# Performance work log

Hardware: AMD Instinct MI355X
Metric: run time of the kernel (lower is better)

Reference implementation:

```python
import jax, jax.numpy as jnp
import numpy as np

NH = 4          # num_heads
EPS = 1e-6
GATE_CAP = 15.0
LOGIT_CAP = 30.0


def soft_cap(x, cap):
    return cap * jnp.tanh(x / cap)


def rms_norm(x, w, eps=EPS):
    xf = x.astype(jnp.float32)
    scale = jax.lax.rsqrt(jnp.mean(xf * xf, axis=-1, keepdims=True) + eps)
    return (xf * scale).astype(x.dtype) * w


def multihead_layernorm(h, w, eps=EPS):
    # h: [B, NH, S, DH]; LayerNorm over DH per head, weight over NH*DH
    hf = h.astype(jnp.float32)
    mu = jnp.mean(hf, axis=-1, keepdims=True)
    var = jnp.mean((hf - mu) ** 2, axis=-1, keepdims=True)
    hn = ((hf - mu) * jax.lax.rsqrt(var + eps)).astype(h.dtype)
    B, nh, S, DH = h.shape
    hn = hn.transpose(0, 2, 1, 3).reshape(B, S, nh * DH)  # [B,S,v_dim]
    return hn * w


def mlstm_parallel(q, k, v, i_pre, f_pre, eps=EPS):
    # q,k: [B,NH,S,Dqk]; v: [B,NH,S,Dv]; i_pre,f_pre: [B,NH,S]
    S = q.shape[2]
    dqk = q.shape[-1]
    logf = jax.nn.log_sigmoid(f_pre.astype(jnp.float32))      # [B,NH,S]
    F = jnp.cumsum(logf, axis=-1)
    # logD[t,s] = F[t] - F[s] + i[s]  for s <= t
    logD = F[..., :, None] - F[..., None, :] + i_pre.astype(jnp.float32)[..., None, :]
    mask = jnp.tril(jnp.ones((S, S), dtype=bool))
    logD = jnp.where(mask, logD, -jnp.inf)
    m = jnp.max(logD, axis=-1, keepdims=True)                  # [B,NH,S,1]
    Dmat = jnp.exp(logD - m)
    scores = jnp.einsum('bhsd,bhtd->bhst', q, k) / jnp.sqrt(float(dqk))
    C = scores * Dmat                                          # [B,NH,S,S]
    n = jnp.maximum(jnp.abs(C.sum(-1)), jnp.exp(-m[..., 0]))   # [B,NH,S]
    h = jnp.einsum('bhst,bhtd->bhsd', C, v) / (n[..., None] + eps)
    return h


def block(x, p):
    (n1, wq, wk, wv, wog, wi, bi, wf, bf, mhw, wout, n2, wg, wu, wd) = p
    B, S, D = x.shape
    xm = rms_norm(x, n1)
    q = xm @ wq.T
    k = xm @ wk.T
    v = xm @ wv.T
    o_pre = xm @ wog.T
    i_pre = soft_cap(xm @ wi.T + bi, GATE_CAP)   # [B,S,NH]
    f_pre = soft_cap(xm @ wf.T + bf, GATE_CAP)
    q = q.reshape(B, S, NH, -1).transpose(0, 2, 1, 3)
    k = k.reshape(B, S, NH, -1).transpose(0, 2, 1, 3)
    v = v.reshape(B, S, NH, -1).transpose(0, 2, 1, 3)
    h = mlstm_parallel(q, k, v, i_pre.transpose(0, 2, 1), f_pre.transpose(0, 2, 1))
    hn = multihead_layernorm(h, mhw)             # [B,S,v_dim]
    y = (hn * jax.nn.sigmoid(o_pre)) @ wout.T
    x = x + y
    xf = rms_norm(x, n2)
    ff = (jax.nn.silu(xf @ wg.T) * (xf @ wu.T)) @ wd.T
    return x + ff


def setup_inputs() -> dict:
    key = jax.random.key(0)
    ks = jax.random.split(key, 16)
    L, D, V, UP, QK = 2, 1024, 32000, 2752, 512
    s = 0.02
    return {
        'tokens': jax.random.randint(ks[0], (1, 2048), 0, V),
        'emb': jax.random.normal(ks[1], (V, D)) * s,
        'norm1_w': jnp.ones((L, D)),
        'Wq': jax.random.normal(ks[2], (L, QK, D)) * s,
        'Wk': jax.random.normal(ks[3], (L, QK, D)) * s,
        'Wv': jax.random.normal(ks[4], (L, D, D)) * s,
        'Wog': jax.random.normal(ks[5], (L, D, D)) * s,
        'Wi': jax.random.normal(ks[6], (L, NH, D)) * s,
        'bi': jax.random.normal(ks[7], (L, NH)) * s,
        'Wf': jax.random.normal(ks[8], (L, NH, D)) * s,
        'bf': jnp.ones((L, NH)) * 3.0,
        'mh_w': jnp.ones((L, D)),
        'Wout': jax.random.normal(ks[9], (L, D, D)) * s,
        'norm2_w': jnp.ones((L, D)),
        'Wg': jax.random.normal(ks[10], (L, UP, D)) * s,
        'Wu': jax.random.normal(ks[11], (L, UP, D)) * s,
        'Wd': jax.random.normal(ks[12], (L, D, UP)) * s,
        'out_norm_w': jnp.ones((D,)),
        'Wlm': jax.random.normal(ks[13], (V, D)) * s,
    }


def reference(tokens, emb, norm1_w, Wq, Wk, Wv, Wog, Wi, bi, Wf, bf, mh_w,
              Wout, norm2_w, Wg, Wu, Wd, out_norm_w, Wlm):
    x = emb[tokens]                    # [B,S,D]
    L = Wq.shape[0]
    for l in range(L):
        p = (norm1_w[l], Wq[l], Wk[l], Wv[l], Wog[l], Wi[l], bi[l], Wf[l],
             bf[l], mh_w[l], Wout[l], norm2_w[l], Wg[l], Wu[l], Wd[l])
        x = block(x, p)
    x = rms_norm(x, out_norm_w)
    logits = x @ Wlm.T
    return soft_cap(logits, LOGIT_CAP)
```

## Files before the change

kernel.cpp:

```cpp
#include <hip/hip_runtime.h>
#include <hip/hip_bf16.h>
#include <math.h>


#define S_LEN 2048
#define DMODEL 1024
#define WLAYER 12845056

typedef __attribute__((ext_vector_type(8))) __bf16 bf16x8;
typedef __attribute__((ext_vector_type(8))) unsigned short u16x8;
typedef __attribute__((ext_vector_type(4))) unsigned short u16x4;
typedef __attribute__((ext_vector_type(4))) float f32x4v;

union cvu { u16x8 u; bf16x8 b; };

__device__ __forceinline__ unsigned short bf_us(float f) {
  union { __bf16 b; unsigned short u; } c;
  c.b = (__bf16)f;
  return c.u;
}
__device__ __forceinline__ float us_f(unsigned short u) {
  union { __bf16 b; unsigned short u; } c;
  c.u = u;
  return (float)c.b;
}
__device__ __forceinline__ bf16x8 ld_bf8(const unsigned short* p, int byte_off) {
  cvu c;
  c.u = *(const u16x8*)((const char*)p + byte_off);
  return c.b;
}
__device__ __forceinline__ float fast_sigmoid(float v) {
  return 1.0f / (1.0f + __expf(-v));
}
__device__ __forceinline__ float fast_softcap30(float v) {
  float e = __expf(-fabsf(v) * (1.0f / 15.0f));
  float t = (1.0f - e) / (1.0f + e);
  return copysignf(30.0f * t, v);
}

#define AS_G __attribute__((address_space(1)))
#define AS_L __attribute__((address_space(3)))

__device__ __forceinline__ void stage64(const unsigned short* gbase, int K,
                                        unsigned short* lds, int wave, int lane, int k0) {
#pragma unroll
  for (int j = 0; j < 4; ++j) {
    const int rbase = (j * 4 + wave) * 8;
    const int r = rbase + (lane >> 3);
    const int cg = (lane & 7) ^ (r & 7);
    const unsigned short* src = gbase + (size_t)r * K + k0 + cg * 8;
    __builtin_amdgcn_global_load_lds((const AS_G void*)src,
                                     (AS_L void*)(lds + rbase * 64), 16, 0, 0);
  }
}

__device__ __forceinline__ void stage32(const unsigned short* gbase, int K,
                                        unsigned short* lds, int wave, int lane, int k0) {
#pragma unroll
  for (int j = 0; j < 2; ++j) {
    const int r = j * 64 + wave * 16 + (lane >> 2);
    const int cg = (lane & 3) ^ ((r >> 1) & 3);
    const unsigned short* src = gbase + (size_t)r * K + k0 + cg * 8;
    __builtin_amdgcn_global_load_lds((const AS_G void*)src,
                                     (AS_L void*)(lds + (j * 64 + wave * 16) * 32), 16, 0, 0);
  }
}

__global__ __launch_bounds__(256) void embed_kernel(
    const int* __restrict__ tok, const float* __restrict__ emb, float* __restrict__ x) {
  int s = blockIdx.x;
  int t = tok[s];
  const float4 v = *(const float4*)(emb + (size_t)t * DMODEL + threadIdx.x * 4);
  *(float4*)(x + (size_t)s * DMODEL + threadIdx.x * 4) = v;
}

__global__ __launch_bounds__(256) void rmsnorm_kernel(
    const float* __restrict__ x, const float* __restrict__ w,
    unsigned short* __restrict__ outb) {
  int s = blockIdx.x, tid = threadIdx.x;
  const float* xr = x + (size_t)s * DMODEL;
  float4 v = *(const float4*)(xr + tid * 4);
  float ss = v.x * v.x + v.y * v.y + v.z * v.z + v.w * v.w;
#pragma unroll
  for (int off = 32; off > 0; off >>= 1) ss += __shfl_down(ss, off);
  __shared__ float red[4];
  if ((tid & 63) == 0) red[tid >> 6] = ss;
  __syncthreads();
  float tot = red[0] + red[1] + red[2] + red[3];
  float scale = rsqrtf(tot * (1.0f / DMODEL) + 1e-6f);
  float4 wv = *(const float4*)(w + tid * 4);
  u16x4 ub;
  ub[0] = bf_us(v.x * scale * wv.x);
  ub[1] = bf_us(v.y * scale * wv.y);
  ub[2] = bf_us(v.z * scale * wv.z);
  ub[3] = bf_us(v.w * scale * wv.w);
  *(u16x4*)(outb + (size_t)s * DMODEL + tid * 4) = ub;
}

__global__ __launch_bounds__(256) void wcvt8_kernel(
    const float* __restrict__ Wq, const float* __restrict__ Wk,
    const float* __restrict__ Wv, const float* __restrict__ Wog,
    const float* __restrict__ Wout, const float* __restrict__ Wg,
    const float* __restrict__ Wu, const float* __restrict__ Wd,
    const float* __restrict__ Wlm,
    unsigned short* __restrict__ W, unsigned short* __restrict__ Wlm16) {
  const size_t de = ((size_t)blockIdx.x * 256 + threadIdx.x) * 8;
  if (de >= 2ull * WLAYER) {
    size_t i = de - 2ull * WLAYER;
    float4 a0 = *(const float4*)(Wlm + i);
    float4 a1 = *(const float4*)(Wlm + i + 4);
    u16x8 o;
    o[0] = bf_us(a0.x); o[1] = bf_us(a0.y); o[2] = bf_us(a0.z); o[3] = bf_us(a0.w);
    o[4] = bf_us(a1.x); o[5] = bf_us(a1.y); o[6] = bf_us(a1.z); o[7] = bf_us(a1.w);
    *(u16x8*)(Wlm16 + i) = o;
    return;
  }
  int e = (int)de, l = 0;
  if (e >= WLAYER) { l = 1; e -= WLAYER; }
  const float* src = nullptr;
  size_t idx = 0;
  if (e < 524288)       { src = Wq  + (size_t)l * 524288;  idx = e; }
  else if (e < 1048576) { src = Wk  + (size_t)l * 524288;  idx = e - 524288; }
  else if (e < 2097152) { src = Wv  + (size_t)l * 1048576; idx = e - 1048576; }
  else if (e < 3145728) { src = Wog + (size_t)l * 1048576; idx = e - 2097152; }
  else if (e < 4194304) { src = Wout + (size_t)l * 1048576; idx = e - 3145728; }
  else if (e < 7077888) {
    int t = e - 4194304, row = t >> 10;
    if (row < 2752) { src = Wg + (size_t)l * 2818048; idx = t; }
  } else if (e < 9961472) {
    int t = e - 7077888, row = t >> 10;
    if (row < 2752) { src = Wu + (size_t)l * 2818048; idx = t; }
  } else {
    int t = e - 9961472, row = t / 2816, col = t - row * 2816;
    if (col < 2752) { src = Wd + (size_t)l * 2818048; idx = row * 2752 + col; }
  }
  u16x8 o;
  if (src) {
    float4 a0 = *(const float4*)(src + idx);
    float4 a1 = *(const float4*)(src + idx + 4);
    o[0] = bf_us(a0.x); o[1] = bf_us(a0.y); o[2] = bf_us(a0.z); o[3] = bf_us(a0.w);
    o[4] = bf_us(a1.x); o[5] = bf_us(a1.y); o[6] = bf_us(a1.z); o[7] = bf_us(a1.w);
  } else {
#pragma unroll
    for (int k = 0; k < 8; ++k) o[k] = 0;
  }
  *(u16x8*)(W + de) = o;
}

template <int EPI>
__global__ __launch_bounds__(256) void gemm_bb_kernel(
    const unsigned short* __restrict__ A, const unsigned short* __restrict__ B,
    const void* Xv, void* Cv, int K, int ldc) {
  __shared__ __align__(16) unsigned short SH[3 * 8192];
  const int tid = threadIdx.x;
  const int wave = tid >> 6, lane = tid & 63;
  const int gx = gridDim.x;
  const int nwg = gx * gridDim.y;
  const int d = blockIdx.y * gx + blockIdx.x;
  const int q = nwg >> 3;
  const int lgc = (d & 7) * q + (d >> 3);
  const int bm = (lgc % gx) * 128, bn = (lgc / gx) * 128;
  const int wr = (wave >> 1) * 64, wc = (wave & 1) * 64;
  const int lr = lane & 15, lhi = lane >> 4;
  const unsigned short* Ab = A + (size_t)bm * K;
  const unsigned short* Bb = B + (size_t)bn * K;
  f32x4v acc[4][4] = {};

  auto stageT = [&](int tau) {
    unsigned short* base = SH + (tau % 3) * 8192;
    stage32(Ab, K, base, wave, lane, tau * 32);
    stage32(Bb, K, base + 4096, wave, lane, tau * 32);
  };

  const int NT = K >> 5;
  stageT(0);
  stageT(1);
  for (int t = 0; t < NT; ++t) {
    if (t < NT - 1) asm volatile("s_waitcnt vmcnt(4)" ::: "memory");
    else            asm volatile("s_waitcnt vmcnt(0)" ::: "memory");
    asm volatile("s_barrier" ::: "memory");
    if (t + 2 < NT) stageT(t + 2);
    const unsigned short* Al = SH + (t % 3) * 8192;
    const unsigned short* Bl = Al + 4096;
    bf16x8 af[4], bfr[4];
#pragma unroll
    for (int mi = 0; mi < 4; ++mi) {
      int row = wr + mi * 16 + lr;
      af[mi] = *(const bf16x8*)&Al[row * 32 + ((lhi ^ ((row >> 1) & 3)) << 3)];
    }
#pragma unroll
    for (int ni = 0; ni < 4; ++ni) {
      int row = wc + ni * 16 + lr;
      bfr[ni] = *(const bf16x8*)&Bl[row * 32 + ((lhi ^ ((row >> 1) & 3)) << 3)];
    }
    __builtin_amdgcn_s_setprio(1);
#pragma unroll
    for (int mi = 0; mi < 4; ++mi)
#pragma unroll
      for (int ni = 0; ni < 4; ++ni)
        acc[mi][ni] = __builtin_amdgcn_mfma_f32_16x16x32_bf16(af[mi], bfr[ni], acc[mi][ni], 0, 0, 0);
    __builtin_amdgcn_s_setprio(0);
  }
#pragma unroll
  for (int mi = 0; mi < 4; ++mi) {
#pragma unroll
    for (int ni = 0; ni < 4; ++ni) {
#pragma unroll
      for (int j = 0; j < 4; ++j) {
        int row = bm + wr + mi * 16 + lhi * 4 + j;
        int col = bn + wc + ni * 16 + lr;
        float v = acc[mi][ni][j];
        if (EPI == 0)
          ((float*)Cv)[(size_t)row * ldc + col] = v;
        if (EPI == 1)
          ((float*)Cv)[(size_t)row * ldc + col] = v + ((const float*)Xv)[(size_t)row * ldc + col];
      }
    }
  }
}

__global__ __launch_bounds__(512, 2) void lm256_kernel(
    const unsigned short* __restrict__ A, const unsigned short* __restrict__ B,
    float* __restrict__ C) {
  __shared__ __align__(16) unsigned short SH[3 * 16384];
  const int K = 1024, N = 32000, NT = 32;
  const int tid = threadIdx.x;
  const int wave = tid >> 6, lane = tid & 63;
  const int lr = lane & 15, lg = lane >> 4;
  const int wm = wave >> 2, wn = wave & 3;
  const int d = blockIdx.y * 8 + blockIdx.x;
  const int lgc = (d & 7) * 125 + (d >> 3);
  const int bm = (lgc & 7) * 256;
  const int bn = (lgc >> 3) * 256;
  const unsigned short* Ab = A + (size_t)bm * K;
  const unsigned short* Bb = B + (size_t)bn * K;

  auto stageM = [&](const unsigned short* gbase, unsigned short* lds, int k0) {
#pragma unroll
    for (int j = 0; j < 2; ++j) {
      const int r = j * 128 + wave * 16 + (lane >> 2);
      const int cg = (lane & 3) ^ ((r >> 1) & 3);
      const unsigned short* src = gbase + (size_t)r * K + k0 + cg * 8;
      __builtin_amdgcn_global_load_lds((const AS_G void*)src,
                                       (AS_L void*)(lds + (j * 128 + wave * 16) * 32), 16, 0, 0);
    }
  };
  auto stageT = [&](int tau) {
    unsigned short* base = SH + (tau % 3) * 16384;
    stageM(Ab, base, tau * 32);
    stageM(Bb, base + 8192, tau * 32);
  };

  f32x4v acc[8][4] = {};
  stageT(0);
  stageT(1);
  for (int t = 0; t < NT; ++t) {
    if (t < NT - 1) asm volatile("s_waitcnt vmcnt(4)" ::: "memory");
    else            asm volatile("s_waitcnt vmcnt(0)" ::: "memory");
    asm volatile("s_barrier" ::: "memory");
    if (t + 2 < NT) stageT(t + 2);
    const unsigned short* Al = SH + (t % 3) * 16384;
    const unsigned short* Bl = Al + 8192;
    bf16x8 bfr[4];
#pragma unroll
    for (int ni = 0; ni < 4; ++ni) {
      int row = wn * 64 + ni * 16 + lr;
      bfr[ni] = *(const bf16x8*)&Bl[row * 32 + ((lg ^ ((row >> 1) & 3)) << 3)];
    }
#pragma unroll
    for (int mi = 0; mi < 8; ++mi) {
      int row = wm * 128 + mi * 16 + lr;
      bf16x8 af = *(const bf16x8*)&Al[row * 32 + ((lg ^ ((row >> 1) & 3)) << 3)];
      __builtin_amdgcn_s_setprio(1);
#pragma unroll
      for (int ni = 0; ni < 4; ++ni)
        acc[mi][ni] = __builtin_amdgcn_mfma_f32_16x16x32_bf16(af, bfr[ni], acc[mi][ni], 0, 0, 0);
      __builtin_amdgcn_s_setprio(0);
    }
  }
#pragma unroll
  for (int mi = 0; mi < 8; ++mi)
#pragma unroll
    for (int ni = 0; ni < 4; ++ni)
#pragma unroll
      for (int jj = 0; jj < 4; ++jj) {
        int row = bm + wm * 128 + mi * 16 + lg * 4 + jj;
        int col = bn + wn * 64 + ni * 16 + lr;
        C[(size_t)row * N + col] = fast_softcap30(acc[mi][ni][jj]);
      }
}

__global__ __launch_bounds__(256) void qkvo_kernel(
    const unsigned short* __restrict__ A, const unsigned short* __restrict__ Wq16,
    const unsigned short* __restrict__ Wk16, const unsigned short* __restrict__ Wv16,
    const unsigned short* __restrict__ Wog16,
    unsigned short* __restrict__ qb, unsigned short* __restrict__ kb,
    unsigned short* __restrict__ vTb, float* __restrict__ og) {
  __shared__ __align__(16) unsigned short SH[3 * 8192];
  const int tid = threadIdx.x;
  const int wave = tid >> 6, lane = tid & 63;
  const int gx = gridDim.x;
  const int nwg = gx * gridDim.y;
  const int dd = blockIdx.y * gx + blockIdx.x;
  const int qq = nwg >> 3;
  const int lgc = (dd & 7) * qq + (dd >> 3);
  const int bm = (lgc % gx) * 128;
  const int by = lgc / gx;
  const unsigned short* B;
  int bnl, mode;
  if (by < 4)       { B = Wq16;  bnl = by * 128;        mode = 0; }
  else if (by < 8)  { B = Wk16;  bnl = (by - 4) * 128;  mode = 1; }
  else if (by < 16) { B = Wv16;  bnl = (by - 8) * 128;  mode = 2; }
  else              { B = Wog16; bnl = (by - 16) * 128; mode = 3; }
  const int K = 1024;
  const int wr = (wave >> 1) * 64, wc = (wave & 1) * 64;
  const int lr = lane & 15, lhi = lane >> 4;
  const unsigned short* Ab = A + (size_t)bm * K;
  const unsigned short* Bb = B + (size_t)bnl * K;
  f32x4v acc[4][4] = {};

  auto stageT = [&](int tau) {
    unsigned short* base = SH + (tau % 3) * 8192;
    stage32(Ab, K, base, wave, lane, tau * 32);
    stage32(Bb, K, base + 4096, wave, lane, tau * 32);
  };

  const int NT = 32;
  stageT(0);
  stageT(1);
  for (int t = 0; t < NT; ++t) {
    if (t < NT - 1) asm volatile("s_waitcnt vmcnt(4)" ::: "memory");
    else            asm volatile("s_waitcnt vmcnt(0)" ::: "memory");
    asm volatile("s_barrier" ::: "memory");
    if (t + 2 < NT) stageT(t + 2);
    const unsigned short* Al = SH + (t % 3) * 8192;
    const unsigned short* Bl = Al + 4096;
    bf16x8 af[4], bfr[4];
#pragma unroll
    for (int mi = 0; mi < 4; ++mi) {
      int row = wr + mi * 16 + lr;
      af[mi] = *(const bf16x8*)&Al[row * 32 + ((lhi ^ ((row >> 1) & 3)) << 3)];
    }
#pragma unroll
    for (int ni = 0; ni < 4; ++ni) {
      int row = wc + ni * 16 + lr;
      bfr[ni] = *(const bf16x8*)&Bl[row * 32 + ((lhi ^ ((row >> 1) & 3)) << 3)];
    }
    __builtin_amdgcn_s_setprio(1);
#pragma unroll
    for (int mi = 0; mi < 4; ++mi)
#pragma unroll
      for (int ni = 0; ni < 4; ++ni)
        acc[mi][ni] = __builtin_amdgcn_mfma_f32_16x16x32_bf16(af[mi], bfr[ni], acc[mi][ni], 0, 0, 0);
    __builtin_amdgcn_s_setprio(0);
  }
  if (mode == 2) {
    __syncthreads();
#pragma unroll
    for (int mi = 0; mi < 4; ++mi)
#pragma unroll
      for (int ni = 0; ni < 4; ++ni)
#pragma unroll
        for (int j = 0; j < 4; ++j) {
          int row = wr + mi * 16 + lhi * 4 + j;
          int col = wc + ni * 16 + lr;
          int byte = col * 256 + ((((row >> 3) ^ (col & 7)) << 4)) + (row & 7) * 2;
          *(unsigned short*)((char*)SH + byte) = bf_us(acc[mi][ni][j]);
        }
    __syncthreads();
#pragma unroll
    for (int i = 0; i < 8; ++i) {
      int c = i * 16 + (tid >> 4);
      int rg = tid & 15;
      u16x8 u = *(const u16x8*)((const char*)SH + c * 256 + ((rg ^ (c & 7)) << 4));
      *(u16x8*)(vTb + (size_t)(bnl + c) * S_LEN + bm + rg * 8) = u;
    }
  } else {
#pragma unroll
    for (int mi = 0; mi < 4; ++mi)
#pragma unroll
      for (int ni = 0; ni < 4; ++ni)
#pragma unroll
        for (int j = 0; j < 4; ++j) {
          int row = bm + wr + mi * 16 + lhi * 4 + j;
          int col = bnl + wc + ni * 16 + lr;
          if (mode == 0)      qb[(size_t)row * 512 + col] = bf_us(acc[mi][ni][j]);
          else if (mode == 1) kb[(size_t)row * 512 + col] = bf_us(acc[mi][ni][j]);
          else                og[(size_t)row * 1024 + col] = acc[mi][ni][j];
        }
  }
}

__global__ __launch_bounds__(256) void ffn_kernel(
    const unsigned short* __restrict__ A, const unsigned short* __restrict__ Bg,
    const unsigned short* __restrict__ Bu, unsigned short* __restrict__ Gb) {
  __shared__ __align__(16) unsigned short As[128 * 64];
  __shared__ __align__(16) unsigned short Bgs[128 * 64];
  __shared__ __align__(16) unsigned short Bus[128 * 64];
  const int K = 1024;
  const int tid = threadIdx.x;
  const int wave = tid >> 6, lane = tid & 63;
  const int gx = gridDim.x;
  const int nwg = gx * gridDim.y;
  const int dd = blockIdx.y * gx + blockIdx.x;
  const int qq = nwg >> 3;
  const int lgc = (dd & 7) * qq + (dd >> 3);
  const int bm = (lgc % gx) * 128;
  const int bn = (lgc / gx) * 128;
  const int wr = (wave >> 1) * 64, wc = (wave & 1) * 64;
  const int lr = lane & 15, lhi = lane >> 4;
  const unsigned short* Ab = A + (size_t)bm * K;
  const unsigned short* Bgb = Bg + (size_t)bn * K;
  const unsigned short* Bub = Bu + (size_t)bn * K;
  f32x4v accg[4][4] = {};
  f32x4v accu[4][4] = {};
  for (int it = 0; it < 16; ++it) {
    stage64(Ab, K, As, wave, lane, it << 6);
    stage64(Bgb, K, Bgs, wave, lane, it << 6);
    stage64(Bub, K, Bus, wave, lane, it << 6);
    __syncthreads();
#pragma unroll
    for (int kk = 0; kk < 2; ++kk) {
      const int sw = (((kk * 4 + lhi) ^ (lr & 7)) << 3);
      bf16x8 af[4], bg[4], bu[4];
#pragma unroll
      for (int mi = 0; mi < 4; ++mi) af[mi] = *(const bf16x8*)&As[(wr + mi * 16 + lr) * 64 + sw];
#pragma unroll
      for (int ni = 0; ni < 4; ++ni) bg[ni] = *(const bf16x8*)&Bgs[(wc + ni * 16 + lr) * 64 + sw];
#pragma unroll
      for (int ni = 0; ni < 4; ++ni) bu[ni] = *(const bf16x8*)&Bus[(wc + ni * 16 + lr) * 64 + sw];
#pragma unroll
      for (int mi = 0; mi < 4; ++mi)
#pragma unroll
        for (int ni = 0; ni < 4; ++ni) {
          accg[mi][ni] = __builtin_amdgcn_mfma_f32_16x16x32_bf16(af[mi], bg[ni], accg[mi][ni], 0, 0, 0);
          accu[mi][ni] = __builtin_amdgcn_mfma_f32_16x16x32_bf16(af[mi], bu[ni], accu[mi][ni], 0, 0, 0);
        }
    }
    __syncthreads();
  }
#pragma unroll
  for (int mi = 0; mi < 4; ++mi) {
#pragma unroll
    for (int ni = 0; ni < 4; ++ni) {
#pragma unroll
      for (int j = 0; j < 4; ++j) {
        int row = bm + wr + mi * 16 + lhi * 4 + j;
        int col = bn + wc + ni * 16 + lr;
        float g = accg[mi][ni][j];
        float sv = g * fast_sigmoid(g) * accu[mi][ni][j];
        Gb[(size_t)row * 2816 + col] = bf_us(sv);
      }
    }
  }
}

__global__ __launch_bounds__(256) void gates_kernel(
    const float* __restrict__ x, const float* __restrict__ n1,
    const float* __restrict__ Wi, const float* __restrict__ bi,
    const float* __restrict__ Wf, const float* __restrict__ bfv,
    float* __restrict__ ipre, float* __restrict__ fpre) {
  int s = blockIdx.x;
  int head = threadIdx.x >> 6, lane = threadIdx.x & 63;
  const float* xr = x + (size_t)s * DMODEL;
  float xv[16];
  float ss = 0.f;
#pragma unroll
  for (int j = 0; j < 16; ++j) { xv[j] = xr[lane + j * 64]; ss += xv[j] * xv[j]; }
#pragma unroll
  for (int off = 32; off > 0; off >>= 1) ss += __shfl_xor(ss, off);
  float scale = rsqrtf(ss * (1.0f / DMODEL) + 1e-6f);
  const float* wi = Wi + head * DMODEL;
  const float* wf = Wf + head * DMODEL;
  float si = 0.f, sf = 0.f;
#pragma unroll
  for (int j = 0; j < 16; ++j) {
    int c = lane + j * 64;
    float xm = xv[j] * scale * n1[c];
    si += xm * wi[c];
    sf += xm * wf[c];
  }
#pragma unroll
  for (int off = 32; off > 0; off >>= 1) {
    si += __shfl_down(si, off);
    sf += __shfl_down(sf, off);
  }
  if (lane == 0) {
    ipre[head * S_LEN + s] = 15.0f * tanhf((si + bi[head]) * (1.0f / 15.0f));
    fpre[head * S_LEN + s] = 15.0f * tanhf((sf + bfv[head]) * (1.0f / 15.0f));
  }
}

__global__ __launch_bounds__(256) void scan_kernel(
    const float* __restrict__ ipre, const float* __restrict__ fpre,
    float* __restrict__ garr, float* __restrict__ Marr, float* __restrict__ earr) {
  const int h = threadIdx.x >> 6;
  const int lane = threadIdx.x & 63;
  const int base = h * S_LEN + lane * 32;
  float lf[32];
  float lsum = 0.f;
#pragma unroll
  for (int e = 0; e < 32; ++e) {
    float f = fpre[base + e];
    float v = fminf(f, 0.f) - log1pf(expf(-fabsf(f)));
    lf[e] = v;
    lsum += v;
  }
  float scan = lsum;
#pragma unroll
  for (int off = 1; off < 64; off <<= 1) {
    float t = __shfl_up(scan, off);
    if (lane >= off) scan += t;
  }
  float F0 = scan - lsum;
  float gv[32];
  float F = F0, lmax = -1e30f;
#pragma unroll
  for (int e = 0; e < 32; ++e) {
    F += lf[e];
    float g = ipre[base + e] - F;
    gv[e] = g;
    lmax = fmaxf(lmax, g);
    garr[base + e] = g;
  }
  float ms = lmax;
#pragma unroll
  for (int off = 1; off < 64; off <<= 1) {
    float t = __shfl_up(ms, off);
    if (lane >= off) ms = fmaxf(ms, t);
  }
  float em = __shfl_up(ms, 1);
  if (lane == 0) em = -1e30f;
  float run = em;
  F = F0;
#pragma unroll
  for (int e = 0; e < 32; ++e) {
    F += lf[e];
    run = fmaxf(run, gv[e]);
    Marr[base + e] = run;
    earr[base + e] = expf(-(F + run));
  }
}

__global__ __launch_bounds__(256) void mlstm_mfma_kernel(
    const unsigned short* __restrict__ Q, const unsigned short* __restrict__ Kb,
    const unsigned short* __restrict__ vT, const float* __restrict__ garr,
    const float* __restrict__ Marr,
    float* __restrict__ hp, float* __restrict__ npart) {
  const int h = blockIdx.y;
  const int T = blockIdx.x;
  const int sp = blockIdx.z;
  float* hpart = hp + (size_t)sp * 2097152;
  const int tid = threadIdx.x;
  const int w = tid >> 6, l = tid & 63;
  const int lr = l & 15, lg = l >> 4;
  const int hbase = h * S_LEN;
  const int sr = tid >> 4;
  const int sc = tid & 15;

  __shared__ __align__(16) unsigned short Ks[64 * 128];
  __shared__ __align__(16) unsigned short Vs[256 * 64];
  __shared__ __align__(16) unsigned short Ps[64 * 64];

  bf16x8 qf[4];
  {
    const unsigned short* qrow = Q + (size_t)(T * 64 + w * 16 + lr) * 512 + h * 128 + lg * 8;
#pragma unroll
    for (int kt = 0; kt < 4; ++kt) {
      cvu c;
      c.u = *(const u16x8*)(qrow + kt * 32);
      qf[kt] = c.b;
    }
  }
  float Mt[4];
#pragma unroll
  for (int j = 0; j < 4; ++j) Mt[j] = Marr[hbase + T * 64 + w * 16 + lg * 4 + j];

  f32x4v pv[16] = {};
  float nacc[4] = {0.f, 0.f, 0.f, 0.f};
  const float rs = 0.08838834764831845f;

  for (int ch = sp; ch <= T; ch += 4) {
    const int s0 = ch * 64;
    __syncthreads();
#pragma unroll
    for (int i = 0; i < 4; ++i) {
      int r = i * 16 + sr;
      u16x8 u = *(const u16x8*)(Kb + (size_t)(s0 + r) * 512 + h * 128 + sc * 8);
      int byte = r * 256 + ((sc * 16) ^ ((r & 7) << 4));
      *(u16x8*)((char*)Ks + byte) = u;
    }
#pragma unroll
    for (int i = 0; i < 16; ++i) {
      int r = i * 16 + sr;
      u16x4 u = *(const u16x4*)(vT + (size_t)(h * 256 + r) * S_LEN + s0 + sc * 4);
      int byte = r * 128 + ((sc * 8) ^ ((r & 7) << 4));
      *(u16x4*)((char*)Vs + byte) = u;
    }
    __syncthreads();
    f32x4v sa[4] = {};
#pragma unroll
    for (int ni = 0; ni < 4; ++ni) {
#pragma unroll
      for (int kt = 0; kt < 4; ++kt) {
        int row = ni * 16 + lr;
        int byte = row * 256 + (((kt * 32 + lg * 8) * 2) ^ ((row & 7) << 4));
        bf16x8 kf = ld_bf8(Ks, byte);
        sa[ni] = __builtin_amdgcn_mfma_f32_16x16x32_bf16(qf[kt], kf, sa[ni], 0, 0, 0);
      }
    }
#pragma unroll
    for (int ni = 0; ni < 4; ++ni) {
      int sl = ni * 16 + lr;
      int sg = s0 + sl;
      float gv = garr[hbase + sg];
#pragma unroll
      for (int j = 0; j < 4; ++j) {
        int tloc = w * 16 + lg * 4 + j;
        int tg = T * 64 + tloc;
        float wgt = (sg <= tg) ? __expf(gv - Mt[j]) : 0.f;
        float val = sa[ni][j] * rs * wgt;
        nacc[j] += val;
        int byte = tloc * 128 + ((sl * 2) ^ ((tloc & 7) << 4));
        *(unsigned short*)((char*)Ps + byte) = bf_us(val);
      }
    }
#pragma unroll
    for (int kt2 = 0; kt2 < 2; ++kt2) {
      int tloc = w * 16 + lr;
      int sb = (kt2 * 32 + lg * 8) * 2;
      bf16x8 pa = ld_bf8(Ps, tloc * 128 + (sb ^ ((tloc & 7) << 4)));
#pragma unroll
      for (int nv = 0; nv < 16; ++nv) {
        int dv = nv * 16 + lr;
        bf16x8 vb = ld_bf8(Vs, dv * 128 + (sb ^ ((dv & 7) << 4)));
        pv[nv] = __builtin_amdgcn_mfma_f32_16x16x32_bf16(pa, vb, pv[nv], 0, 0, 0);
      }
    }
  }
#pragma unroll
  for (int j = 0; j < 4; ++j) {
#pragma unroll
    for (int off = 1; off < 16; off <<= 1) nacc[j] += __shfl_xor(nacc[j], off);
  }
#pragma unroll
  for (int j = 0; j < 4; ++j) {
    int tg = T * 64 + w * 16 + lg * 4 + j;
    if (lr == 0) npart[sp * 8192 + hbase + tg] = nacc[j];
    float* orow = hpart + (size_t)tg * DMODEL + h * 256;
#pragma unroll
    for (int nvt = 0; nvt < 16; ++nvt) orow[nvt * 16 + lr] = pv[nvt][j];
  }
}

__global__ __launch_bounds__(256) void mhln_gate_kernel(
    const float* __restrict__ hp, const float* __restrict__ npart,
    const float* __restrict__ earr, const float* __restrict__ mhw,
    const float* __restrict__ og, unsigned short* __restrict__ gact) {
  int s = blockIdx.x;
  int head = threadIdx.x >> 6, lane = threadIdx.x & 63;
  float n = (npart[head * S_LEN + s] + npart[8192 + head * S_LEN + s]) +
            (npart[16384 + head * S_LEN + s] + npart[24576 + head * S_LEN + s]);
  float nvv = fmaxf(fabsf(n), earr[head * S_LEN + s]);
  float inv = 1.0f / (nvv + 1e-6f);
  const size_t base = (size_t)s * DMODEL + head * 256;
  float vq[4];
#pragma unroll
  for (int qy = 0; qy < 4; ++qy) {
    size_t o = base + qy * 64 + lane;
    vq[qy] = ((hp[o] + hp[o + 2097152]) + (hp[o + 4194304] + hp[o + 6291456])) * inv;
  }
  float sum = vq[0] + vq[1] + vq[2] + vq[3];
#pragma unroll
  for (int off = 32; off > 0; off >>= 1) sum += __shfl_xor(sum, off);
  float mu = sum * (1.0f / 256.0f);
  float d0 = vq[0] - mu, d1 = vq[1] - mu, d2 = vq[2] - mu, d3 = vq[3] - mu;
  float vs = d0 * d0 + d1 * d1 + d2 * d2 + d3 * d3;
#pragma unroll
  for (int off = 32; off > 0; off >>= 1) vs += __shfl_xor(vs, off);
  float rstd = rsqrtf(vs * (1.0f / 256.0f) + 1e-6f);
  float dn[4] = {d0, d1, d2, d3};
#pragma unroll
  for (int qy = 0; qy < 4; ++qy) {
    int c = head * 256 + qy * 64 + lane;
    float ov = og[(size_t)s * DMODEL + c];
    gact[(size_t)s * DMODEL + c] = bf_us(dn[qy] * rstd * mhw[c] * fast_sigmoid(ov));
  }
}

extern "C" void kernel_launch(void* const* d_in, const int* in_sizes, int n_in,
                              void* d_out, int out_size, void* d_ws, size_t ws_size,
                              hipStream_t stream) {
  (void)in_sizes; (void)n_in; (void)out_size; (void)ws_size;
  const int*   tok   = (const int*)d_in[0];
  const float* emb   = (const float*)d_in[1];
  const float* norm1 = (const float*)d_in[2];
  const float* Wq    = (const float*)d_in[3];
  const float* Wk    = (const float*)d_in[4];
  const float* Wv    = (const float*)d_in[5];
  const float* Wog   = (const float*)d_in[6];
  const float* Wi    = (const float*)d_in[7];
  const float* bi    = (const float*)d_in[8];
  const float* Wf    = (const float*)d_in[9];
  const float* bfp   = (const float*)d_in[10];
  const float* mhw   = (const float*)d_in[11];
  const float* Wout  = (const float*)d_in[12];
  const float* norm2 = (const float*)d_in[13];
  const float* Wg    = (const float*)d_in[14];
  const float* Wu    = (const float*)d_in[15];
  const float* Wd    = (const float*)d_in[16];
  const float* onw   = (const float*)d_in[17];
  const float* Wlm   = (const float*)d_in[18];

  char* wsb = (char*)d_ws;
  const size_t MB = 1ull << 20;
  float*          x    = (float*)wsb;
  unsigned short* xmb  = (unsigned short*)(wsb + 8 * MB);
  float*          ipre = (float*)(wsb + 12 * MB);
  float*          fpre = ipre + 8192;
  float*          garr = fpre + 8192;
  float*          Marr = garr + 8192;
  float*          earr = Marr + 8192;
  float*          npart = earr + 8192;
  unsigned short* W16  = (unsigned short*)(wsb + 13 * MB);
  const size_t OQ = 0, OKk = 524288, OV = 1048576, OOG = 2097152, OOUT = 3145728,
               OGt = 4194304, OU = 7077888, OD = 9961472;
  unsigned short* qb    = (unsigned short*)(wsb + 62 * MB);
  unsigned short* kb    = (unsigned short*)(wsb + 64 * MB);
  unsigned short* vTb   = (unsigned short*)(wsb + 66 * MB);
  float*          og    = (float*)(wsb + 70 * MB);
  float*          hp    = (float*)(wsb + 78 * MB);
  unsigned short* gact  = (unsigned short*)(wsb + 110 * MB);
  unsigned short* Gb16  = (unsigned short*)(wsb + 114 * MB);
  unsigned short* wlm16 = (unsigned short*)(wsb + 126 * MB);

  embed_kernel<<<2048, 256, 0, stream>>>(tok, emb, x);
  wcvt8_kernel<<<28544, 256, 0, stream>>>(Wq, Wk, Wv, Wog, Wout, Wg, Wu, Wd, Wlm,
                                          W16, wlm16);

  for (int l = 0; l < 2; ++l) {
    const unsigned short* Wl = W16 + (size_t)l * WLAYER;
    const float* n1   = norm1 + (size_t)l * 1024;
    const float* wiv  = Wi   + (size_t)l * 4 * 1024;
    const float* bil  = bi   + (size_t)l * 4;
    const float* wfv  = Wf   + (size_t)l * 4 * 1024;
    const float* bfl  = bfp  + (size_t)l * 4;
    const float* mhwl = mhw  + (size_t)l * 1024;
    const float* n2   = norm2 + (size_t)l * 1024;

    rmsnorm_kernel<<<2048, 256, 0, stream>>>(x, n1, xmb);
    qkvo_kernel<<<dim3(16, 24), 256, 0, stream>>>(xmb, Wl + OQ, Wl + OKk, Wl + OV,
                                                  Wl + OOG, qb, kb, vTb, og);
    gates_kernel<<<2048, 256, 0, stream>>>(x, n1, wiv, bil, wfv, bfl, ipre, fpre);
    scan_kernel<<<1, 256, 0, stream>>>(ipre, fpre, garr, Marr, earr);
    mlstm_mfma_kernel<<<dim3(32, 4, 4), 256, 0, stream>>>(qb, kb, vTb, garr, Marr,
                                                          hp, npart);
    mhln_gate_kernel<<<2048, 256, 0, stream>>>(hp, npart, earr, mhwl, og, gact);
    gemm_bb_kernel<1><<<dim3(16, 8), 256, 0, stream>>>(gact, Wl + OOUT, x, x, 1024, 1024);
    rmsnorm_kernel<<<2048, 256, 0, stream>>>(x, n2, xmb);
    ffn_kernel<<<dim3(16, 22), 256, 0, stream>>>(xmb, Wl + OGt, Wl + OU, Gb16);
    gemm_bb_kernel<1><<<dim3(16, 8), 256, 0, stream>>>(Gb16, Wl + OD, x, x, 2816, 1024);
  }

  rmsnorm_kernel<<<2048, 256, 0, stream>>>(x, onw, xmb);
  lm256_kernel<<<dim3(8, 125), 512, 0, stream>>>(xmb, wlm16, (float*)d_out);
}
```

Measured before the change: 731.3 us.

## Triple-buffer FFN gate/up GEMM with K=32 stages and async prefetch

The fused gate/up FFN kernel moves from a single-buffered K=64 loop with two block barriers per step to a triple-buffered K=32 pipeline. Tiles are prefetched two steps ahead through global_load_lds, and each step waits only on the oldest outstanding loads with a manual vmcnt wait plus one barrier. MFMA sections are bracketed with s_setprio. The aim is to hide global-load latency behind matrix math and remove one barrier per iteration, at the cost of more shared memory (72KB), which can lower occupancy.

```diff
diff --git a/kernel.cpp b/kernel.cpp
--- a/kernel.cpp
+++ b/kernel.cpp
@@ -40,19 +40,6 @@
 
 #define AS_G __attribute__((address_space(1)))
 #define AS_L __attribute__((address_space(3)))
-
-__device__ __forceinline__ void stage64(const unsigned short* gbase, int K,
-                                        unsigned short* lds, int wave, int lane, int k0) {
-#pragma unroll
-  for (int j = 0; j < 4; ++j) {
-    const int rbase = (j * 4 + wave) * 8;
-    const int r = rbase + (lane >> 3);
-    const int cg = (lane & 7) ^ (r & 7);
-    const unsigned short* src = gbase + (size_t)r * K + k0 + cg * 8;
-    __builtin_amdgcn_global_load_lds((const AS_G void*)src,
-                                     (AS_L void*)(lds + rbase * 64), 16, 0, 0);
-  }
-}
 
 __device__ __forceinline__ void stage32(const unsigned short* gbase, int K,
                                         unsigned short* lds, int wave, int lane, int k0) {
@@ -394,9 +381,7 @@
 __global__ __launch_bounds__(256) void ffn_kernel(
     const unsigned short* __restrict__ A, const unsigned short* __restrict__ Bg,
     const unsigned short* __restrict__ Bu, unsigned short* __restrict__ Gb) {
-  __shared__ __align__(16) unsigned short As[128 * 64];
-  __shared__ __align__(16) unsigned short Bgs[128 * 64];
-  __shared__ __align__(16) unsigned short Bus[128 * 64];
+  __shared__ __align__(16) unsigned short SH[3 * 12288];
   const int K = 1024;
   const int tid = threadIdx.x;
   const int wave = tid >> 6, lane = tid & 63;
@@ -414,30 +399,47 @@
   const unsigned short* Bub = Bu + (size_t)bn * K;
   f32x4v accg[4][4] = {};
   f32x4v accu[4][4] = {};
-  for (int it = 0; it < 16; ++it) {
-    stage64(Ab, K, As, wave, lane, it << 6);
-    stage64(Bgb, K, Bgs, wave, lane, it << 6);
-    stage64(Bub, K, Bus, wave, lane, it << 6);
-    __syncthreads();
-#pragma unroll
-    for (int kk = 0; kk < 2; ++kk) {
-      const int sw = (((kk * 4 + lhi) ^ (lr & 7)) << 3);
-      bf16x8 af[4], bg[4], bu[4];
-#pragma unroll
-      for (int mi = 0; mi < 4; ++mi) af[mi] = *(const bf16x8*)&As[(wr + mi * 16 + lr) * 64 + sw];
-#pragma unroll
-      for (int ni = 0; ni < 4; ++ni) bg[ni] = *(const bf16x8*)&Bgs[(wc + ni * 16 + lr) * 64 + sw];
-#pragma unroll
-      for (int ni = 0; ni < 4; ++ni) bu[ni] = *(const bf16x8*)&Bus[(wc + ni * 16 + lr) * 64 + sw];
-#pragma unroll
-      for (int mi = 0; mi < 4; ++mi)
-#pragma unroll
-        for (int ni = 0; ni < 4; ++ni) {
-          accg[mi][ni] = __builtin_amdgcn_mfma_f32_16x16x32_bf16(af[mi], bg[ni], accg[mi][ni], 0, 0, 0);
-          accu[mi][ni] = __builtin_amdgcn_mfma_f32_16x16x32_bf16(af[mi], bu[ni], accu[mi][ni], 0, 0, 0);
-        }
-    }
-    __syncthreads();
+
+  auto stageT = [&](int tau) {
+    unsigned short* base = SH + (tau % 3) * 12288;
+    stage32(Ab, K, base, wave, lane, tau * 32);
+    stage32(Bgb, K, base + 4096, wave, lane, tau * 32);
+    stage32(Bub, K, base + 8192, wave, lane, tau * 32);
+  };
+
+  const int NT = 32;
+  stageT(0);
+  stageT(1);
+  for (int t = 0; t < NT; ++t) {
+    if (t < NT - 1) asm volatile("s_waitcnt vmcnt(6)" ::: "memory");
+    else            asm volatile("s_waitcnt vmcnt(0)" ::: "memory");
+    asm volatile("s_barrier" ::: "memory");
+    if (t + 2 < NT) stageT(t + 2);
+    const unsigned short* Al = SH + (t % 3) * 12288;
+    const unsigned short* Bgl = Al + 4096;
+    const unsigned short* Bul = Al + 8192;
+    bf16x8 af[4], bg[4], bu[4];
+#pragma unroll
+    for (int mi = 0; mi < 4; ++mi) {
+      int row = wr + mi * 16 + lr;
+      af[mi] = *(const bf16x8*)&Al[row * 32 + ((lhi ^ ((row >> 1) & 3)) << 3)];
+    }
+#pragma unroll
+    for (int ni = 0; ni < 4; ++ni) {
+      int row = wc + ni * 16 + lr;
+      int sw = ((lhi ^ ((row >> 1) & 3)) << 3);
+      bg[ni] = *(const bf16x8*)&Bgl[row * 32 + sw];
+      bu[ni] = *(const bf16x8*)&Bul[row * 32 + sw];
+    }
+    __builtin_amdgcn_s_setprio(1);
+#pragma unroll
+    for (int mi = 0; mi < 4; ++mi)
+#pragma unroll
+      for (int ni = 0; ni < 4; ++ni) {
+        accg[mi][ni] = __builtin_amdgcn_mfma_f32_16x16x32_bf16(af[mi], bg[ni], accg[mi][ni], 0, 0, 0);
+        accu[mi][ni] = __builtin_amdgcn_mfma_f32_16x16x32_bf16(af[mi], bu[ni], accu[mi][ni], 0, 0, 0);
+      }
+    __builtin_amdgcn_s_setprio(0);
   }
 #pragma unroll
   for (int mi = 0; mi < 4; ++mi) {
```

New measurement: 724.2 us. No clear change (-1.0%).
